# Optimization experiments

Measured on AMD Instinct MI355X. Metric: run time of the kernel, lower is better.

The kernel has to match this reference:

```python
import jax, jax.numpy as jnp
import numpy as np

MAX_CLUSTERS = 5
CLUSTER_SIZE_MAX = 3
K_HOP = 2
TAU = 1.0  # epoch=0 -> tau_init * decay^0 = 1.0
NEG = -1e9


def _logits(x, ctx, W1, b1, W2, b2):
    # x: [B,N,D], ctx: [B,H] -> logits [B,N] (selection_mlp, dropout=eval/identity)
    B, N, _ = x.shape
    h = jnp.concatenate([x, jnp.broadcast_to(ctx[:, None, :], (B, N, ctx.shape[-1]))], axis=-1)
    h = jax.nn.relu(h @ W1.T + b1)
    return (h @ W2.T + b2)[..., 0]


def _select(logits, cand, key):
    # Hard Gumbel-Softmax argmax over candidate nodes; zeros row if no candidates.
    any_c = cand.any(axis=-1, keepdims=True)
    ml = jnp.where(cand, logits, NEG)
    u = jax.random.uniform(key, logits.shape, dtype=logits.dtype)
    g = -jnp.log(-jnp.log(u + 1e-8) + 1e-8)
    idx = jnp.argmax((ml + g) / TAU, axis=-1)
    oh = jax.nn.one_hot(idx, logits.shape[-1], dtype=logits.dtype)
    return oh * any_c.astype(logits.dtype)


def _gru(seq, h0, Wih, Whh, bih, bhh):
    # torch nn.GRU single layer, batch_first; seq: [B,T,D], h0: [B,H] -> final hidden [B,H]
    def cell(h, xt):
        gi = xt @ Wih.T + bih
        gh = h @ Whh.T + bhh
        ir, iz, inn = jnp.split(gi, 3, axis=-1)
        hr, hz, hn = jnp.split(gh, 3, axis=-1)
        r = jax.nn.sigmoid(ir + hr)
        z = jax.nn.sigmoid(iz + hz)
        n = jnp.tanh(inn + r * hn)
        return (1.0 - z) * n + z * h, None
    h, _ = jax.lax.scan(cell, h0, jnp.swapaxes(seq, 0, 1))
    return h


def reference(x, adj, mask, W1, b1, W2, b2, Wc, bc, Wih, Whh, bih, bhh):
    B, N, D = x.shape
    key = jax.random.key(42)
    avail = mask.astype(bool)
    ctx = x.mean(axis=1) @ Wc.T + bc          # context_init  [B,H]
    h_gru = jnp.zeros_like(ctx)               # context_hidden
    assign = jnp.zeros((B, N, MAX_CLUSTERS), x.dtype)
    embs, hist = [], []
    for c in range(MAX_CLUSTERS):
        # logits are identical for every selection within this cluster (same x, same context)
        logits = _logits(x, ctx, W1, b1, W2, b2)  # [B,N]
        # seed selection (torch uses .item() -> selection is a constant index; no grad path)
        seed = jax.lax.stop_gradient(_select(logits, avail, jax.random.fold_in(key, 2 * c)))
        avail = avail & ~(seed > 0.5)
        # k-hop BFS from seed via adjacency matvecs
        reach = seed > 0.5
        cur = seed
        for _ in range(K_HOP):
            nb = jnp.einsum('bn,bnm->bm', cur, adj) > 0
            new = nb & ~reach
            reach = reach | nb
            cur = new.astype(x.dtype)
        member = seed
        for a in range(CLUSTER_SIZE_MAX - 1):
            cand = avail & reach
            sel = jax.lax.stop_gradient(_select(logits, cand, jax.random.fold_in(key, 2 * c + 1000 + a)))
            avail = avail & ~(sel > 0.5)
            member = member + sel
        assign = assign.at[:, :, c].set(member)
        cnt = member.sum(axis=-1, keepdims=True)
        emb = jnp.einsum('bn,bnd->bd', member, x) / jnp.maximum(cnt, 1.0)  # mean of member feats; 0 if empty
        embs.append(emb)
        hist.append(emb)
        # torch re-runs the GRU over the FULL cluster history each iteration, starting
        # from the previously updated hidden state (faithful to the original code)
        h_gru = _gru(jnp.stack(hist, axis=1), h_gru, Wih, Whh, bih, bhh)
        ctx = h_gru
    cluster_features = jnp.stack(embs, axis=1)               # [B,S,D]
    S = MAX_CLUSTERS
    cluster_adj = jnp.ones((B, S, S), x.dtype) - jnp.eye(S, dtype=x.dtype)[None]
    return cluster_features, cluster_adj, assign


def setup_inputs() -> dict:
    key = jax.random.key(0)
    ks = jax.random.split(key, 10)
    B, N, D, H = 16, 2048, 128, 64
    x = jax.random.normal(ks[0], (B, N, D), dtype=jnp.float32)
    # sparse symmetric binary adjacency, ~16 neighbors per node
    a = (jax.random.uniform(ks[1], (B, N, N)) < 0.004).astype(jnp.float32)
    adj = jnp.clip(a + jnp.swapaxes(a, 1, 2), 0.0, 1.0)
    adj = adj * (1.0 - jnp.eye(N, dtype=jnp.float32)[None])
    mask = jnp.ones((B, N), dtype=jnp.int32)
    s = 0.05
    return {
        'x': x, 'adj': adj, 'mask': mask,
        'W1': jax.random.normal(ks[2], (H, D + H)) * s, 'b1': jnp.zeros((H,)),
        'W2': jax.random.normal(ks[3], (1, H)) * s, 'b2': jnp.zeros((1,)),
        'Wc': jax.random.normal(ks[4], (H, D)) * s, 'bc': jnp.zeros((H,)),
        'Wih': jax.random.normal(ks[5], (3 * H, D)) * s,
        'Whh': jax.random.normal(ks[6], (3 * H, H)) * s,
        'bih': jnp.zeros((3 * H,)), 'bhh': jnp.zeros((3 * H,)),
    }
```

## Files before the change

kernel.cpp:

```cpp
#include <hip/hip_runtime.h>
#include <cfloat>
#include <cmath>

#define NB 2048
#define BB 16
#define DD 128
#define HH 64
#define MAXC 5
#define CSMAX 3
#define NT 1024

__device__ __forceinline__ unsigned rotl32(unsigned v, int d) {
  return (v << d) | (v >> (32 - d));
}

__device__ __forceinline__ void tf2x32(unsigned k0, unsigned k1, unsigned x0, unsigned x1,
                                       unsigned& o0, unsigned& o1) {
  unsigned ks2 = k0 ^ k1 ^ 0x1BD11BDAu;
  x0 += k0; x1 += k1;
#define RND(r) { x0 += x1; x1 = rotl32(x1, r); x1 ^= x0; }
  RND(13) RND(15) RND(26) RND(6)   x0 += k1;  x1 += ks2 + 1u;
  RND(17) RND(29) RND(16) RND(24)  x0 += ks2; x1 += k0 + 2u;
  RND(13) RND(15) RND(26) RND(6)   x0 += k0;  x1 += k1 + 3u;
  RND(17) RND(29) RND(16) RND(24)  x0 += k1;  x1 += ks2 + 4u;
  RND(13) RND(15) RND(26) RND(6)   x0 += ks2; x1 += k0 + 5u;
#undef RND
  o0 = x0; o1 = x1;
}

__device__ __forceinline__ float gumbel_for(unsigned k0, unsigned k1, unsigned idx) {
  unsigned o0, o1;
  tf2x32(k0, k1, 0u, idx, o0, o1);
  unsigned bits = o0 ^ o1;
  float u = __uint_as_float((bits >> 9) | 0x3f800000u) - 1.0f;
  float uu = u + 1e-8f;
  return -logf(-logf(uu) + 1e-8f);
}

__global__ __launch_bounds__(NT) void gvp_prep(
    const float* __restrict__ x, const float* __restrict__ W1,
    float* __restrict__ P, float* __restrict__ partial, float* __restrict__ gumb) {
  __shared__ __align__(16) float s_W1[HH][DD + 4];
  __shared__ float sp[8][DD];
  const int bid = blockIdx.x, tid = threadIdx.x;

  if (bid < 128) {
    for (int i = tid; i < HH * (DD / 4); i += NT) {
      int r = i >> 5, q = i & 31;
      *(float4*)&s_W1[r][q * 4] = *(const float4*)(W1 + (size_t)r * (DD + HH) + q * 4);
    }
    __syncthreads();
    const int jg = tid & 15, ng = tid >> 4;
    const int j0 = jg * 4;
    const size_t n0 = (size_t)bid * 256 + ng * 4;
    const float4* x4 = (const float4*)x;
    float acc[4][4];
#pragma unroll
    for (int i = 0; i < 4; i++)
#pragma unroll
      for (int q = 0; q < 4; q++) acc[i][q] = 0.f;
    for (int kq = 0; kq < 32; kq++) {
      float4 xv[4], wv[4];
#pragma unroll
      for (int i = 0; i < 4; i++) xv[i] = x4[(n0 + i) * 32 + kq];
#pragma unroll
      for (int q = 0; q < 4; q++) wv[q] = *(const float4*)&s_W1[j0 + q][kq * 4];
#pragma unroll
      for (int i = 0; i < 4; i++)
#pragma unroll
        for (int q = 0; q < 4; q++)
          acc[i][q] += xv[i].x * wv[q].x + xv[i].y * wv[q].y +
                       xv[i].z * wv[q].z + xv[i].w * wv[q].w;
    }
#pragma unroll
    for (int i = 0; i < 4; i++)
#pragma unroll
      for (int q = 0; q < 4; q++)
        P[(n0 + i) * HH + j0 + q] = acc[i][q];
  } else if (bid < 384) {
    const int bm = bid - 128;
    const int b = bm >> 4, chunk = bm & 15;
    const int d = tid & (DD - 1), part = tid >> 7;
    float acc = 0.f;
    const int base = chunk * 128 + part;
#pragma unroll
    for (int k = 0; k < 16; k++)
      acc += x[((size_t)b * NB + base + k * 8) * DD + d];
    sp[part][d] = acc;
    __syncthreads();
    if (tid < DD) {
      float m = 0.f;
#pragma unroll
      for (int p = 0; p < 8; p++) m += sp[p][tid];
      partial[((size_t)b * 16 + chunk) * DD + tid] = m;
    }
  } else {
    const int bg = bid - 384;
    const int base = (bg * NT + tid) * 4;
#pragma unroll
    for (int i = 0; i < 4; i++) {
      int idx = base + i;
      int sel = idx >> 15;
      int rem = idx & 32767;
      int c = sel / 3, s = sel - 3 * c;
      unsigned data = (s == 0) ? (unsigned)(2 * c) : (unsigned)(2 * c + 1000 + (s - 1));
      unsigned k0, k1;
      tf2x32(0u, 42u, 0u, data, k0, k1);
      gumb[idx] = gumbel_for(k0, k1, (unsigned)rem);
    }
  }
}

__global__ __launch_bounds__(NT, 4) void gvp_main(
    const float* __restrict__ x, const float* __restrict__ adj, const int* __restrict__ mask,
    const float* __restrict__ W1, const float* __restrict__ b1,
    const float* __restrict__ W2, const float* __restrict__ b2,
    const float* __restrict__ Wc, const float* __restrict__ bc,
    const float* __restrict__ Wih, const float* __restrict__ Whh,
    const float* __restrict__ bih, const float* __restrict__ bhh,
    const float* __restrict__ P, const float* __restrict__ partial,
    const float* __restrict__ gumb,
    float* __restrict__ out_feat, float* __restrict__ out_adjm, float* __restrict__ out_assign) {
  const int b = blockIdx.x;
  const int tid = threadIdx.x;

  __shared__ __align__(16) float s_logits[NB];
  __shared__ __align__(16) float s_gumb[2][NB];
  __shared__ unsigned char s_avail[NB], s_reach[NB], s_assignB[NB];
  __shared__ short s_list[128];
  __shared__ int s_cnt;
  __shared__ unsigned long long s_key[CSMAX];
  __shared__ __align__(16) float s_ctx[HH], s_q[HH];
  __shared__ __align__(16) float s_h[2][HH];
  __shared__ __align__(16) float s_hist[MAXC][DD];
  __shared__ __align__(16) float s_giAll[MAXC][3 * HH];
  __shared__ __align__(16) float s_Whh[3 * HH][HH + 4];
  __shared__ __align__(16) float s_W1c[HH][HH + 4];
  __shared__ __align__(16) float s_W2[HH];
  __shared__ float s_bhh[3 * HH], s_b1[HH];
  __shared__ __align__(16) float s_mean[DD];
  __shared__ float s_b2v;

  const size_t xb = (size_t)b * NB * DD;
  const float4* adj4 = (const float4*)(adj + (size_t)b * NB * NB);
  const float4* P4 = (const float4*)(P + (size_t)b * NB * HH);

  auto scanReduce = [&](float bv, int bi, int slot) {
#pragma unroll
    for (int off = 32; off; off >>= 1) {
      float ov = __shfl_down(bv, off);
      int oi = __shfl_down(bi, off);
      if (ov > bv || (ov == bv && oi < bi)) { bv = ov; bi = oi; }
    }
    if ((tid & 63) == 0 && bi < NB) {
      unsigned u = __float_as_uint(bv);
      u = (u & 0x80000000u) ? ~u : (u | 0x80000000u);
      unsigned long long key = ((unsigned long long)u << 32) | (unsigned)(~bi);
      atomicMax(&s_key[slot], key);
    }
  };
  auto decodeIdx = [](unsigned long long k) -> int {
    return k ? (int)(unsigned)(~(unsigned)k) : -1;
  };

  for (int i = tid; i < 3 * HH * (HH / 4); i += NT) {
    int r = i >> 4, q = i & 15;
    *(float4*)&s_Whh[r][q * 4] = *(const float4*)(Whh + (size_t)r * HH + q * 4);
  }
  {
    int r = tid >> 4, q = tid & 15;
    *(float4*)&s_W1c[r][q * 4] = *(const float4*)(W1 + (size_t)r * (DD + HH) + DD + q * 4);
  }
  if (tid < 3 * HH) s_bhh[tid] = bhh[tid];
  if (tid < HH) { s_W2[tid] = W2[tid]; s_b1[tid] = b1[tid]; s_h[0][tid] = 0.f; }
  if (tid == 0) s_b2v = b2[0];
#pragma unroll
  for (int r = 0; r < 2; r++) {
    int n = tid + r * NT;
    s_avail[n] = (mask[b * NB + n] != 0) ? 1 : 0;
    s_assignB[n] = 0;
  }
  if (tid < DD) {
    float m = 0.f;
#pragma unroll
    for (int k = 0; k < 16; k++) m += partial[((size_t)b * 16 + k) * DD + tid];
    s_mean[tid] = m * (1.0f / NB);
  }
  __syncthreads();
  if (tid < 4 * HH) {
    int row = tid >> 2, g = tid & 3;
    const float4* wr = (const float4*)(Wc + (size_t)row * DD) + g * 8;
    const float4* m4 = (const float4*)s_mean + g * 8;
    float s = 0.f;
#pragma unroll
    for (int i = 0; i < 8; i++) {
      float4 w = wr[i], m = m4[i];
      s += w.x * m.x + w.y * m.y + w.z * m.z + w.w * m.w;
    }
    s += __shfl_xor(s, 1);
    s += __shfl_xor(s, 2);
    if (g == 0) s_ctx[row] = s + bc[row];
  }
  __syncthreads();

  int hp = 0;

  for (int c = 0; c < MAXC; c++) {
    const float* g0p = gumb + ((size_t)(c * 3) * BB + b) * NB;
    const float4* g12 = (const float4*)(gumb + ((size_t)(c * 3 + 1 + (tid >> 9)) * BB + b) * NB);
    float4 gst = g12[tid & 511];
    const int n0 = tid, n1 = tid + NT;
    float gs0 = g0p[n0], gs1 = g0p[n1];
    ((float4*)s_gumb)[tid] = gst;
    if (tid < 4 * HH) {
      int row = tid >> 2, g = tid & 3;
      const float4* wr = (const float4*)&s_W1c[row][0] + g * 4;
      const float4* c4 = (const float4*)s_ctx + g * 4;
      float s = 0.f;
#pragma unroll
      for (int i = 0; i < 4; i++) {
        float4 w = wr[i], cc = c4[i];
        s += w.x * cc.x + w.y * cc.y + w.z * cc.z + w.w * cc.w;
      }
      s += __shfl_xor(s, 1);
      s += __shfl_xor(s, 2);
      if (g == 0) s_q[row] = s + s_b1[row];
    }
    if (tid < CSMAX) s_key[tid] = 0ull;
    if (tid == 0) s_cnt = 0;
    __syncthreads();

    {
      float l0 = s_b2v, l1 = s_b2v;
      const float4* p0 = P4 + (size_t)n0 * 16;
      const float4* p1 = P4 + (size_t)n1 * 16;
      const float4* q4 = (const float4*)s_q;
      const float4* w4 = (const float4*)s_W2;
#pragma unroll
      for (int qq = 0; qq < 16; qq += 4) {
        float4 A[4], Bv[4];
#pragma unroll
        for (int i = 0; i < 4; i++) { A[i] = p0[qq + i]; Bv[i] = p1[qq + i]; }
#pragma unroll
        for (int i = 0; i < 4; i++) {
          float4 qv = q4[qq + i], w = w4[qq + i];
          l0 += w.x * fmaxf(A[i].x + qv.x, 0.f) + w.y * fmaxf(A[i].y + qv.y, 0.f) +
                w.z * fmaxf(A[i].z + qv.z, 0.f) + w.w * fmaxf(A[i].w + qv.w, 0.f);
          l1 += w.x * fmaxf(Bv[i].x + qv.x, 0.f) + w.y * fmaxf(Bv[i].y + qv.y, 0.f) +
                w.z * fmaxf(Bv[i].z + qv.z, 0.f) + w.w * fmaxf(Bv[i].w + qv.w, 0.f);
        }
      }
      s_logits[n0] = l0;
      s_logits[n1] = l1;
      float bv = -FLT_MAX;
      int bi = NB;
      if (s_avail[n0]) { float y = l0 + gs0; if (y > bv) { bv = y; bi = n0; } }
      if (s_avail[n1]) { float y = l1 + gs1; if (y > bv || (y == bv && n1 < bi)) { bv = y; bi = n1; } }
      scanReduce(bv, bi, 0);
    }
    __syncthreads();

    const int seed = decodeIdx(s_key[0]);
    if (tid < 512) {
      if (seed >= 0) {
        float4 a = adj4[(size_t)seed * 512 + tid];
        int m = tid << 2;
        unsigned f0 = a.x > 0.f, f1 = a.y > 0.f, f2 = a.z > 0.f, f3 = a.w > 0.f;
        unsigned r = f0 | (f1 << 8) | (f2 << 16) | (f3 << 24);
        if ((seed >> 2) == tid) r |= 1u << ((seed & 3) * 8);
        ((unsigned*)s_reach)[tid] = r;
        if (f0 && m != seed)     { int p = atomicAdd(&s_cnt, 1); if (p < 128) s_list[p] = (short)m; }
        if (f1 && m + 1 != seed) { int p = atomicAdd(&s_cnt, 1); if (p < 128) s_list[p] = (short)(m + 1); }
        if (f2 && m + 2 != seed) { int p = atomicAdd(&s_cnt, 1); if (p < 128) s_list[p] = (short)(m + 2); }
        if (f3 && m + 3 != seed) { int p = atomicAdd(&s_cnt, 1); if (p < 128) s_list[p] = (short)(m + 3); }
      } else {
        ((unsigned*)s_reach)[tid] = 0u;
      }
    }
    __syncthreads();

    if (seed >= 0) {
      int cnt = min(s_cnt, 128);
      int m4 = tid & 511, rg = tid >> 9;
      bool a0 = false, a1 = false, a2 = false, a3 = false;
#pragma unroll
      for (int k = 0; k < 20; k++) {
        int li = rg + 2 * k;
        if (li < cnt) {
          int n = s_list[li];
          float4 a = adj4[(size_t)n * 512 + m4];
          a0 |= a.x > 0.f; a1 |= a.y > 0.f; a2 |= a.z > 0.f; a3 |= a.w > 0.f;
        }
      }
      for (int li = rg + 40; li < cnt; li += 2) {
        int n = s_list[li];
        float4 a = adj4[(size_t)n * 512 + m4];
        a0 |= a.x > 0.f; a1 |= a.y > 0.f; a2 |= a.z > 0.f; a3 |= a.w > 0.f;
      }
      int m = m4 << 2;
      if (a0) s_reach[m] = 1;
      if (a1) s_reach[m + 1] = 1;
      if (a2) s_reach[m + 2] = 1;
      if (a3) s_reach[m + 3] = 1;
    }
    __syncthreads();

    {
      float bv = -FLT_MAX;
      int bi = NB;
#pragma unroll
      for (int r = 0; r < 2; r++) {
        int n = tid + r * NT;
        if (s_avail[n] && s_reach[n] && n != seed) {
          float y = s_logits[n] + s_gumb[0][n];
          if (y > bv || (y == bv && n < bi)) { bv = y; bi = n; }
        }
      }
      scanReduce(bv, bi, 1);
    }
    __syncthreads();

    const int w1i = decodeIdx(s_key[1]);
    {
      float bv = -FLT_MAX;
      int bi = NB;
#pragma unroll
      for (int r = 0; r < 2; r++) {
        int n = tid + r * NT;
        if (s_avail[n] && s_reach[n] && n != seed && n != w1i) {
          float y = s_logits[n] + s_gumb[1][n];
          if (y > bv || (y == bv && n < bi)) { bv = y; bi = n; }
        }
      }
      scanReduce(bv, bi, 2);
    }
    __syncthreads();

    const int w2i = decodeIdx(s_key[2]);
    {
      int mc = (seed >= 0) + (w1i >= 0) + (w2i >= 0);
      if (tid < DD) {
        float acc = 0.f;
        if (seed >= 0) acc += x[xb + (size_t)seed * DD + tid];
        if (w1i >= 0) acc += x[xb + (size_t)w1i * DD + tid];
        if (w2i >= 0) acc += x[xb + (size_t)w2i * DD + tid];
        float e = acc / fmaxf((float)mc, 1.0f);
        s_hist[c][tid] = e;
        out_feat[((size_t)b * MAXC + c) * DD + tid] = e;
      } else if (tid >= 128 && tid < 128 + CSMAX) {
        int idx = (tid == 128) ? seed : (tid == 129 ? w1i : w2i);
        if (idx >= 0) { s_avail[idx] = 0; s_assignB[idx] |= (unsigned char)(1 << c); }
      }
    }
    __syncthreads();

    if (tid < 4 * 3 * HH) {
      int row = tid >> 2, g = tid & 3;
      const float4* wr = (const float4*)(Wih + (size_t)row * DD) + g * 8;
      const float4* h4 = (const float4*)s_hist[c] + g * 8;
      float s = 0.f;
#pragma unroll
      for (int i = 0; i < 8; i++) {
        float4 w = wr[i], hh = h4[i];
        s += w.x * hh.x + w.y * hh.y + w.z * hh.z + w.w * hh.w;
      }
      s += __shfl_xor(s, 1);
      s += __shfl_xor(s, 2);
      if (g == 0) s_giAll[c][row] = s + bih[row];
    }
    __syncthreads();

    for (int t0 = 0; t0 <= c; t0++) {
      if (tid < 4 * HH) {
        int row = tid >> 2, g = tid & 3;
        const float4* h4 = (const float4*)s_h[hp] + g * 4;
        float4 hv[4];
#pragma unroll
        for (int i = 0; i < 4; i++) hv[i] = h4[i];
        const float4* wr = (const float4*)&s_Whh[row][0] + g * 4;
        const float4* wz = (const float4*)&s_Whh[HH + row][0] + g * 4;
        const float4* wn = (const float4*)&s_Whh[2 * HH + row][0] + g * 4;
        float sr = 0.f, sz = 0.f, sn = 0.f;
#pragma unroll
        for (int i = 0; i < 4; i++) {
          float4 a = wr[i], bz = wz[i], cn = wn[i], h = hv[i];
          sr += a.x * h.x + a.y * h.y + a.z * h.z + a.w * h.w;
          sz += bz.x * h.x + bz.y * h.y + bz.z * h.z + bz.w * h.w;
          sn += cn.x * h.x + cn.y * h.y + cn.z * h.z + cn.w * h.w;
        }
        sr += __shfl_xor(sr, 1); sr += __shfl_xor(sr, 2);
        sz += __shfl_xor(sz, 1); sz += __shfl_xor(sz, 2);
        sn += __shfl_xor(sn, 1); sn += __shfl_xor(sn, 2);
        if (g == 0) {
          float r = 1.f / (1.f + expf(-(s_giAll[t0][row] + sr + s_bhh[row])));
          float z = 1.f / (1.f + expf(-(s_giAll[t0][HH + row] + sz + s_bhh[HH + row])));
          float nn = tanhf(s_giAll[t0][2 * HH + row] + r * (sn + s_bhh[2 * HH + row]));
          float hn = (1.f - z) * nn + z * s_h[hp][row];
          s_h[hp ^ 1][row] = hn;
          if (t0 == c) s_ctx[row] = hn;
        }
      }
      hp ^= 1;
      __syncthreads();
    }
  }

#pragma unroll
  for (int r = 0; r < 2; r++) {
    int n = tid + r * NT;
    unsigned bits = s_assignB[n];
    size_t base = ((size_t)(b * NB + n)) * MAXC;
#pragma unroll
    for (int cc = 0; cc < MAXC; cc++)
      out_assign[base + cc] = (float)((bits >> cc) & 1u);
  }
  for (int i = tid; i < MAXC * MAXC; i += NT)
    out_adjm[(size_t)b * MAXC * MAXC + i] = ((i / MAXC) == (i % MAXC)) ? 0.f : 1.f;
}

extern "C" void kernel_launch(void* const* d_in, const int* in_sizes, int n_in,
                              void* d_out, int out_size, void* d_ws, size_t ws_size,
                              hipStream_t stream) {
  const float* x   = (const float*)d_in[0];
  const float* adj = (const float*)d_in[1];
  const int*   mask= (const int*)d_in[2];
  const float* W1  = (const float*)d_in[3];
  const float* b1  = (const float*)d_in[4];
  const float* W2  = (const float*)d_in[5];
  const float* b2  = (const float*)d_in[6];
  const float* Wc  = (const float*)d_in[7];
  const float* bc  = (const float*)d_in[8];
  const float* Wih = (const float*)d_in[9];
  const float* Whh = (const float*)d_in[10];
  const float* bih = (const float*)d_in[11];
  const float* bhh = (const float*)d_in[12];

  float* ws = (float*)d_ws;
  float* P       = ws;
  float* partial = P + (size_t)BB * NB * HH;
  float* gumb    = partial + (size_t)BB * 16 * DD;

  float* out = (float*)d_out;
  float* out_feat = out;
  float* out_adjm = out + (size_t)BB * MAXC * DD;
  float* out_assign = out_adjm + (size_t)BB * MAXC * MAXC;

  hipLaunchKernelGGL(gvp_prep, dim3(504), dim3(NT), 0, stream, x, W1, P, partial, gumb);
  hipLaunchKernelGGL(gvp_main, dim3(BB), dim3(NT), 0, stream,
                     x, adj, mask, W1, b1, W2, b2, Wc, bc, Wih, Whh, bih, bhh, P, partial, gumb,
                     out_feat, out_adjm, out_assign);
}
```

Baseline: 195.0 us.

## Compute Gumbel noise in main kernel and merge member selections into one top-2 pass

The prep kernel no longer precomputes Gumbel noise into a workspace buffer. The main kernel now generates the noise inline with Threefry and computes both member picks in a single pass using a warp top-2 reduction, which removes a block-wide reduction and several barriers per cluster. The GRU input projection is fused with the embedding sum and the per-cluster scaling, and the GRU recurrence runs in a single wavefront using transposed weights. This trades global traffic and synchronisation for extra ALU work and puts the serial GRU steps on 64 threads. The top-2 pass drops the old explicit exclusion of the seed and first pick from the second member's candidates; it relies on the seed already being marked unavailable and on skipping the first pick by index.

Measured after the change: 326.9 us. +67.6%, slower.

```diff
diff --git a/kernel.cpp b/kernel.cpp
--- a/kernel.cpp
+++ b/kernel.cpp
@@ -7,8 +7,10 @@
 #define DD 128
 #define HH 64
 #define MAXC 5
-#define CSMAX 3
 #define NT 1024
+
+#define OFF_P 0
+#define OFF_PART (OFF_P + BB * NB * HH)
 
 __device__ __forceinline__ unsigned rotl32(unsigned v, int d) {
   return (v << d) | (v >> (32 - d));
@@ -37,15 +39,25 @@
   return -logf(-logf(uu) + 1e-8f);
 }
 
-__global__ __launch_bounds__(NT) void gvp_prep(
-    const float* __restrict__ x, const float* __restrict__ W1,
-    float* __restrict__ P, float* __restrict__ partial, float* __restrict__ gumb) {
+__device__ __forceinline__ unsigned long long packKey(float y, int n) {
+  unsigned u = __float_as_uint(y);
+  u = (u & 0x80000000u) ? ~u : (u | 0x80000000u);
+  return ((unsigned long long)u << 32) | (unsigned)(~(unsigned)n);
+}
+__device__ __forceinline__ int decodeKey(unsigned long long k) {
+  return k ? (int)(~(unsigned)k) : -1;
+}
+
+__global__ __launch_bounds__(1024) void gvp_prep(
+    const float* __restrict__ x, const float* __restrict__ W1, float* __restrict__ ws) {
   __shared__ __align__(16) float s_W1[HH][DD + 4];
   __shared__ float sp[8][DD];
   const int bid = blockIdx.x, tid = threadIdx.x;
+  float* P = ws + OFF_P;
+  float* partial = ws + OFF_PART;
 
   if (bid < 128) {
-    for (int i = tid; i < HH * (DD / 4); i += NT) {
+    for (int i = tid; i < HH * (DD / 4); i += 1024) {
       int r = i >> 5, q = i & 31;
       *(float4*)&s_W1[r][q * 4] = *(const float4*)(W1 + (size_t)r * (DD + HH) + q * 4);
     }
@@ -77,7 +89,7 @@
 #pragma unroll
       for (int q = 0; q < 4; q++)
         P[(n0 + i) * HH + j0 + q] = acc[i][q];
-  } else if (bid < 384) {
+  } else {
     const int bm = bid - 128;
     const int b = bm >> 4, chunk = bm & 15;
     const int d = tid & (DD - 1), part = tid >> 7;
@@ -93,20 +105,6 @@
 #pragma unroll
       for (int p = 0; p < 8; p++) m += sp[p][tid];
       partial[((size_t)b * 16 + chunk) * DD + tid] = m;
-    }
-  } else {
-    const int bg = bid - 384;
-    const int base = (bg * NT + tid) * 4;
-#pragma unroll
-    for (int i = 0; i < 4; i++) {
-      int idx = base + i;
-      int sel = idx >> 15;
-      int rem = idx & 32767;
-      int c = sel / 3, s = sel - 3 * c;
-      unsigned data = (s == 0) ? (unsigned)(2 * c) : (unsigned)(2 * c + 1000 + (s - 1));
-      unsigned k0, k1;
-      tf2x32(0u, 42u, 0u, data, k0, k1);
-      gumb[idx] = gumbel_for(k0, k1, (unsigned)rem);
     }
   }
 }
@@ -118,75 +116,54 @@
     const float* __restrict__ Wc, const float* __restrict__ bc,
     const float* __restrict__ Wih, const float* __restrict__ Whh,
     const float* __restrict__ bih, const float* __restrict__ bhh,
-    const float* __restrict__ P, const float* __restrict__ partial,
-    const float* __restrict__ gumb,
+    const float* __restrict__ ws,
     float* __restrict__ out_feat, float* __restrict__ out_adjm, float* __restrict__ out_assign) {
   const int b = blockIdx.x;
   const int tid = threadIdx.x;
-
-  __shared__ __align__(16) float s_logits[NB];
-  __shared__ __align__(16) float s_gumb[2][NB];
-  __shared__ unsigned char s_avail[NB], s_reach[NB], s_assignB[NB];
-  __shared__ short s_list[128];
+  const int t = tid;
+
+  __shared__ float s_WhhT[HH][3 * HH];
+  __shared__ float s_W1cT[HH][HH];
+  __shared__ unsigned char s_avail[NB], s_assignB[NB];
+  __shared__ short s_flist[128];
   __shared__ int s_cnt;
-  __shared__ unsigned long long s_key[CSMAX];
-  __shared__ __align__(16) float s_ctx[HH], s_q[HH];
-  __shared__ __align__(16) float s_h[2][HH];
-  __shared__ __align__(16) float s_hist[MAXC][DD];
+  __shared__ unsigned long long s_key[2];
+  __shared__ unsigned long long s_top2[16][2];
   __shared__ __align__(16) float s_giAll[MAXC][3 * HH];
-  __shared__ __align__(16) float s_Whh[3 * HH][HH + 4];
-  __shared__ __align__(16) float s_W1c[HH][HH + 4];
-  __shared__ __align__(16) float s_W2[HH];
-  __shared__ float s_bhh[3 * HH], s_b1[HH];
+  __shared__ __align__(16) float s_h[HH], s_q[HH], s_ctx[HH];
   __shared__ __align__(16) float s_mean[DD];
+  __shared__ float s_bhh[3 * HH], s_b1[HH], s_W2v[HH];
   __shared__ float s_b2v;
 
+  const size_t adjb = (size_t)b * NB * NB;
   const size_t xb = (size_t)b * NB * DD;
-  const float4* adj4 = (const float4*)(adj + (size_t)b * NB * NB);
-  const float4* P4 = (const float4*)(P + (size_t)b * NB * HH);
-
-  auto scanReduce = [&](float bv, int bi, int slot) {
-#pragma unroll
-    for (int off = 32; off; off >>= 1) {
-      float ov = __shfl_down(bv, off);
-      int oi = __shfl_down(bi, off);
-      if (ov > bv || (ov == bv && oi < bi)) { bv = ov; bi = oi; }
-    }
-    if ((tid & 63) == 0 && bi < NB) {
-      unsigned u = __float_as_uint(bv);
-      u = (u & 0x80000000u) ? ~u : (u | 0x80000000u);
-      unsigned long long key = ((unsigned long long)u << 32) | (unsigned)(~bi);
-      atomicMax(&s_key[slot], key);
-    }
-  };
-  auto decodeIdx = [](unsigned long long k) -> int {
-    return k ? (int)(unsigned)(~(unsigned)k) : -1;
-  };
-
-  for (int i = tid; i < 3 * HH * (HH / 4); i += NT) {
-    int r = i >> 4, q = i & 15;
-    *(float4*)&s_Whh[r][q * 4] = *(const float4*)(Whh + (size_t)r * HH + q * 4);
-  }
-  {
-    int r = tid >> 4, q = tid & 15;
-    *(float4*)&s_W1c[r][q * 4] = *(const float4*)(W1 + (size_t)r * (DD + HH) + DD + q * 4);
+  const float4* P4 = (const float4*)(ws + OFF_P) + (size_t)b * NB * 16;
+
+  for (int f = tid; f < HH * 3 * HH; f += NT) {
+    int k = f / (3 * HH), row = f - k * (3 * HH);
+    s_WhhT[k][row] = Whh[(size_t)row * HH + k];
+  }
+  for (int f = tid; f < HH * HH; f += NT) {
+    int k = f >> 6, row = f & (HH - 1);
+    s_W1cT[k][row] = W1[(size_t)row * (DD + HH) + DD + k];
   }
   if (tid < 3 * HH) s_bhh[tid] = bhh[tid];
-  if (tid < HH) { s_W2[tid] = W2[tid]; s_b1[tid] = b1[tid]; s_h[0][tid] = 0.f; }
+  if (tid >= 256 && tid < 256 + HH) s_b1[tid - 256] = b1[tid - 256];
+  if (tid >= 320 && tid < 320 + HH) s_W2v[tid - 320] = W2[tid - 320];
+  s_avail[t] = (mask[b * NB + t] != 0) ? 1 : 0;
+  s_avail[t + NT] = (mask[b * NB + t + NT] != 0) ? 1 : 0;
+  s_assignB[t] = 0;
+  s_assignB[t + NT] = 0;
+  if (tid >= 384 && tid < 384 + DD) {
+    int d = tid - 384;
+    float m = 0.f;
+#pragma unroll
+    for (int k = 0; k < 16; k++) m += ws[OFF_PART + ((size_t)b * 16 + k) * DD + d];
+    s_mean[d] = m * (1.0f / NB);
+  }
   if (tid == 0) s_b2v = b2[0];
-#pragma unroll
-  for (int r = 0; r < 2; r++) {
-    int n = tid + r * NT;
-    s_avail[n] = (mask[b * NB + n] != 0) ? 1 : 0;
-    s_assignB[n] = 0;
-  }
-  if (tid < DD) {
-    float m = 0.f;
-#pragma unroll
-    for (int k = 0; k < 16; k++) m += partial[((size_t)b * 16 + k) * DD + tid];
-    s_mean[tid] = m * (1.0f / NB);
-  }
   __syncthreads();
+
   if (tid < 4 * HH) {
     int row = tid >> 2, g = tid & 3;
     const float4* wr = (const float4*)(Wc + (size_t)row * DD) + g * 8;
@@ -203,219 +180,224 @@
   }
   __syncthreads();
 
-  int hp = 0;
+  if (tid < 64) {
+    int r = tid;
+    float qs = 0.f;
+    for (int k = 0; k < HH; k += 4) {
+      float4 cv = *(const float4*)&s_ctx[k];
+      qs += s_W1cT[k][r] * cv.x + s_W1cT[k + 1][r] * cv.y +
+            s_W1cT[k + 2][r] * cv.z + s_W1cT[k + 3][r] * cv.w;
+    }
+    s_q[r] = qs + s_b1[r];
+    s_h[r] = 0.f;
+  } else if (tid < 66) s_key[tid - 64] = 0ull;
+  else if (tid < 98) ((unsigned long long*)s_top2)[tid - 66] = 0ull;
+  else if (tid == 98) s_cnt = 0;
+  __syncthreads();
+
+  float l0, l1;
 
   for (int c = 0; c < MAXC; c++) {
-    const float* g0p = gumb + ((size_t)(c * 3) * BB + b) * NB;
-    const float4* g12 = (const float4*)(gumb + ((size_t)(c * 3 + 1 + (tid >> 9)) * BB + b) * NB);
-    float4 gst = g12[tid & 511];
-    const int n0 = tid, n1 = tid + NT;
-    float gs0 = g0p[n0], gs1 = g0p[n1];
-    ((float4*)s_gumb)[tid] = gst;
-    if (tid < 4 * HH) {
-      int row = tid >> 2, g = tid & 3;
-      const float4* wr = (const float4*)&s_W1c[row][0] + g * 4;
-      const float4* c4 = (const float4*)s_ctx + g * 4;
-      float s = 0.f;
-#pragma unroll
-      for (int i = 0; i < 4; i++) {
-        float4 w = wr[i], cc = c4[i];
-        s += w.x * cc.x + w.y * cc.y + w.z * cc.z + w.w * cc.w;
-      }
-      s += __shfl_xor(s, 1);
-      s += __shfl_xor(s, 2);
-      if (g == 0) s_q[row] = s + s_b1[row];
-    }
-    if (tid < CSMAX) s_key[tid] = 0ull;
-    if (tid == 0) s_cnt = 0;
-    __syncthreads();
-
     {
-      float l0 = s_b2v, l1 = s_b2v;
-      const float4* p0 = P4 + (size_t)n0 * 16;
-      const float4* p1 = P4 + (size_t)n1 * 16;
-      const float4* q4 = (const float4*)s_q;
-      const float4* w4 = (const float4*)s_W2;
-#pragma unroll
-      for (int qq = 0; qq < 16; qq += 4) {
-        float4 A[4], Bv[4];
-#pragma unroll
-        for (int i = 0; i < 4; i++) { A[i] = p0[qq + i]; Bv[i] = p1[qq + i]; }
-#pragma unroll
-        for (int i = 0; i < 4; i++) {
-          float4 qv = q4[qq + i], w = w4[qq + i];
-          l0 += w.x * fmaxf(A[i].x + qv.x, 0.f) + w.y * fmaxf(A[i].y + qv.y, 0.f) +
-                w.z * fmaxf(A[i].z + qv.z, 0.f) + w.w * fmaxf(A[i].w + qv.w, 0.f);
-          l1 += w.x * fmaxf(Bv[i].x + qv.x, 0.f) + w.y * fmaxf(Bv[i].y + qv.y, 0.f) +
-                w.z * fmaxf(Bv[i].z + qv.z, 0.f) + w.w * fmaxf(Bv[i].w + qv.w, 0.f);
+      unsigned ka, kb;
+      tf2x32(0u, 42u, 0u, (unsigned)(2 * c), ka, kb);
+      const float4* p0 = P4 + (size_t)t * 16;
+      const float4* p1 = P4 + (size_t)(t + NT) * 16;
+      l0 = s_b2v;
+      l1 = s_b2v;
+#pragma unroll
+      for (int i = 0; i < 16; i++) {
+        float4 pa = p0[i], pb = p1[i];
+        float4 qv = *(const float4*)&s_q[i * 4];
+        float4 w = *(const float4*)&s_W2v[i * 4];
+        l0 += w.x * fmaxf(pa.x + qv.x, 0.f) + w.y * fmaxf(pa.y + qv.y, 0.f) +
+              w.z * fmaxf(pa.z + qv.z, 0.f) + w.w * fmaxf(pa.w + qv.w, 0.f);
+        l1 += w.x * fmaxf(pb.x + qv.x, 0.f) + w.y * fmaxf(pb.y + qv.y, 0.f) +
+              w.z * fmaxf(pb.z + qv.z, 0.f) + w.w * fmaxf(pb.w + qv.w, 0.f);
+      }
+      unsigned long long key = 0ull;
+      if (s_avail[t]) key = packKey(l0 + gumbel_for(ka, kb, (unsigned)(b * NB + t)), t);
+      if (s_avail[t + NT]) {
+        unsigned long long k2 =
+            packKey(l1 + gumbel_for(ka, kb, (unsigned)(b * NB + t + NT)), t + NT);
+        if (k2 > key) key = k2;
+      }
+#pragma unroll
+      for (int off = 32; off; off >>= 1) {
+        unsigned long long o = __shfl_down(key, off);
+        if (o > key) key = o;
+      }
+      if ((tid & 63) == 0 && key) atomicMax(&s_key[0], key);
+    }
+    __syncthreads();
+
+    const int seed = decodeKey(s_key[0]);
+    bool r0 = false, r1 = false;
+    if (seed >= 0) {
+      const float* srow = adj + adjb + (size_t)seed * NB;
+      float a0v = srow[t], a1v = srow[t + NT];
+      r0 = a0v > 0.f;
+      r1 = a1v > 0.f;
+      if (r0) { int p = atomicAdd(&s_cnt, 1); if (p < 128) s_flist[p] = (short)t; }
+      if (r1) { int p = atomicAdd(&s_cnt, 1); if (p < 128) s_flist[p] = (short)(t + NT); }
+      r0 |= (t == seed);
+      r1 |= (t + NT == seed);
+      if (tid == 0) s_avail[seed] = 0;
+    }
+    unsigned k1a, k1b, k2a, k2b;
+    tf2x32(0u, 42u, 0u, (unsigned)(2 * c + 1000), k1a, k1b);
+    tf2x32(0u, 42u, 0u, (unsigned)(2 * c + 1001), k2a, k2b);
+    float g1a = gumbel_for(k1a, k1b, (unsigned)(b * NB + t));
+    float g1b = gumbel_for(k1a, k1b, (unsigned)(b * NB + t + NT));
+    float g2a = gumbel_for(k2a, k2b, (unsigned)(b * NB + t));
+    float g2b = gumbel_for(k2a, k2b, (unsigned)(b * NB + t + NT));
+    __syncthreads();
+
+    if (seed >= 0) {
+      int fc = min(s_cnt, 128);
+      const float* ab = adj + adjb;
+      int fi = 0;
+      for (; fi + 2 <= fc; fi += 2) {
+        int ra = s_flist[fi], rb = s_flist[fi + 1];
+        float a0 = ab[(size_t)ra * NB + t], a1 = ab[(size_t)ra * NB + t + NT];
+        float c0 = ab[(size_t)rb * NB + t], c1 = ab[(size_t)rb * NB + t + NT];
+        r0 |= (a0 > 0.f) | (c0 > 0.f);
+        r1 |= (a1 > 0.f) | (c1 > 0.f);
+      }
+      if (fi < fc) {
+        int ra = s_flist[fi];
+        r0 |= ab[(size_t)ra * NB + t] > 0.f;
+        r1 |= ab[(size_t)ra * NB + t + NT] > 0.f;
+      }
+    }
+    {
+      bool c0 = r0 && s_avail[t], c1 = r1 && s_avail[t + NT];
+      unsigned long long key1 = 0ull, ta = 0ull, tb = 0ull;
+      if (c0) {
+        key1 = packKey(l0 + g1a, t);
+        ta = packKey(l0 + g2a, t);
+      }
+      if (c1) {
+        unsigned long long k = packKey(l1 + g1b, t + NT);
+        if (k > key1) key1 = k;
+        unsigned long long k2 = packKey(l1 + g2b, t + NT);
+        if (k2 > ta) { tb = ta; ta = k2; } else tb = k2;
+      }
+#pragma unroll
+      for (int off = 32; off; off >>= 1) {
+        unsigned long long o = __shfl_down(key1, off);
+        if (o > key1) key1 = o;
+        unsigned long long o1 = __shfl_down(ta, off);
+        unsigned long long o2 = __shfl_down(tb, off);
+        unsigned long long lo = ta < o1 ? ta : o1;
+        unsigned long long hi2 = tb > o2 ? tb : o2;
+        ta = ta > o1 ? ta : o1;
+        tb = lo > hi2 ? lo : hi2;
+      }
+      if ((tid & 63) == 0) {
+        if (key1) atomicMax(&s_key[1], key1);
+        s_top2[tid >> 6][0] = ta;
+        s_top2[tid >> 6][1] = tb;
+      }
+    }
+    __syncthreads();
+
+    const int w1 = decodeKey(s_key[1]);
+    int w2;
+    {
+      unsigned long long t1 = 0ull, t2 = 0ull;
+#pragma unroll
+      for (int i = 0; i < 32; i++) {
+        unsigned long long k = ((unsigned long long*)s_top2)[i];
+        if (k > t1) { t2 = t1; t1 = k; } else if (k > t2) t2 = k;
+      }
+      int i1 = decodeKey(t1);
+      w2 = (i1 == w1) ? decodeKey(t2) : i1;
+    }
+    {
+      int mc = (seed >= 0) + (w1 >= 0) + (w2 >= 0);
+      float invmc = 1.0f / fmaxf((float)mc, 1.0f);
+      if (c < MAXC - 1 && tid < 768) {
+        int row = tid >> 2, g = tid & 3;
+        const float4* wr = (const float4*)(Wih + (size_t)row * DD) + g * 8;
+        const float4* x0 = (seed >= 0) ? (const float4*)(x + xb + (size_t)seed * DD) + g * 8 : nullptr;
+        const float4* x1 = (w1 >= 0) ? (const float4*)(x + xb + (size_t)w1 * DD) + g * 8 : nullptr;
+        const float4* x2 = (w2 >= 0) ? (const float4*)(x + xb + (size_t)w2 * DD) + g * 8 : nullptr;
+        float s = 0.f;
+#pragma unroll
+        for (int i = 0; i < 8; i++) {
+          float4 w = wr[i];
+          float sx = 0.f, sy = 0.f, sz = 0.f, sw = 0.f;
+          if (x0) { float4 v = x0[i]; sx += v.x; sy += v.y; sz += v.z; sw += v.w; }
+          if (x1) { float4 v = x1[i]; sx += v.x; sy += v.y; sz += v.z; sw += v.w; }
+          if (x2) { float4 v = x2[i]; sx += v.x; sy += v.y; sz += v.z; sw += v.w; }
+          s += w.x * sx + w.y * sy + w.z * sz + w.w * sw;
         }
-      }
-      s_logits[n0] = l0;
-      s_logits[n1] = l1;
-      float bv = -FLT_MAX;
-      int bi = NB;
-      if (s_avail[n0]) { float y = l0 + gs0; if (y > bv) { bv = y; bi = n0; } }
-      if (s_avail[n1]) { float y = l1 + gs1; if (y > bv || (y == bv && n1 < bi)) { bv = y; bi = n1; } }
-      scanReduce(bv, bi, 0);
-    }
-    __syncthreads();
-
-    const int seed = decodeIdx(s_key[0]);
-    if (tid < 512) {
-      if (seed >= 0) {
-        float4 a = adj4[(size_t)seed * 512 + tid];
-        int m = tid << 2;
-        unsigned f0 = a.x > 0.f, f1 = a.y > 0.f, f2 = a.z > 0.f, f3 = a.w > 0.f;
-        unsigned r = f0 | (f1 << 8) | (f2 << 16) | (f3 << 24);
-        if ((seed >> 2) == tid) r |= 1u << ((seed & 3) * 8);
-        ((unsigned*)s_reach)[tid] = r;
-        if (f0 && m != seed)     { int p = atomicAdd(&s_cnt, 1); if (p < 128) s_list[p] = (short)m; }
-        if (f1 && m + 1 != seed) { int p = atomicAdd(&s_cnt, 1); if (p < 128) s_list[p] = (short)(m + 1); }
-        if (f2 && m + 2 != seed) { int p = atomicAdd(&s_cnt, 1); if (p < 128) s_list[p] = (short)(m + 2); }
-        if (f3 && m + 3 != seed) { int p = atomicAdd(&s_cnt, 1); if (p < 128) s_list[p] = (short)(m + 3); }
-      } else {
-        ((unsigned*)s_reach)[tid] = 0u;
-      }
-    }
-    __syncthreads();
-
-    if (seed >= 0) {
-      int cnt = min(s_cnt, 128);
-      int m4 = tid & 511, rg = tid >> 9;
-      bool a0 = false, a1 = false, a2 = false, a3 = false;
-#pragma unroll
-      for (int k = 0; k < 20; k++) {
-        int li = rg + 2 * k;
-        if (li < cnt) {
-          int n = s_list[li];
-          float4 a = adj4[(size_t)n * 512 + m4];
-          a0 |= a.x > 0.f; a1 |= a.y > 0.f; a2 |= a.z > 0.f; a3 |= a.w > 0.f;
+        s += __shfl_xor(s, 1);
+        s += __shfl_xor(s, 2);
+        if (g == 0) s_giAll[c][row] = s * invmc + bih[row];
+      }
+      if (tid >= 768 && tid < 768 + DD) {
+        int d = tid - 768;
+        float acc = 0.f;
+        if (seed >= 0) acc += x[xb + (size_t)seed * DD + d];
+        if (w1 >= 0) acc += x[xb + (size_t)w1 * DD + d];
+        if (w2 >= 0) acc += x[xb + (size_t)w2 * DD + d];
+        out_feat[((size_t)b * MAXC + c) * DD + d] = acc * invmc;
+      }
+      if (tid == 896 && seed >= 0) s_assignB[seed] |= (unsigned char)(1 << c);
+      if (tid == 897 && w1 >= 0) { s_assignB[w1] |= (unsigned char)(1 << c); s_avail[w1] = 0; }
+      if (tid == 898 && w2 >= 0) { s_assignB[w2] |= (unsigned char)(1 << c); s_avail[w2] = 0; }
+    }
+    __syncthreads();
+
+    if (c < MAXC - 1) {
+      if (tid < 64) {
+        const int r = tid;
+        float h = s_h[r];
+        for (int tt = 0; tt <= c; tt++) {
+          float sr = 0.f, sz = 0.f, sn = 0.f;
+          for (int k = 0; k < HH; k += 4) {
+            float4 hv = *(const float4*)&s_h[k];
+            sr += s_WhhT[k][r] * hv.x + s_WhhT[k + 1][r] * hv.y +
+                  s_WhhT[k + 2][r] * hv.z + s_WhhT[k + 3][r] * hv.w;
+            sz += s_WhhT[k][HH + r] * hv.x + s_WhhT[k + 1][HH + r] * hv.y +
+                  s_WhhT[k + 2][HH + r] * hv.z + s_WhhT[k + 3][HH + r] * hv.w;
+            sn += s_WhhT[k][2 * HH + r] * hv.x + s_WhhT[k + 1][2 * HH + r] * hv.y +
+                  s_WhhT[k + 2][2 * HH + r] * hv.z + s_WhhT[k + 3][2 * HH + r] * hv.w;
+          }
+          float rr = 1.f / (1.f + expf(-(s_giAll[tt][r] + sr + s_bhh[r])));
+          float zz = 1.f / (1.f + expf(-(s_giAll[tt][HH + r] + sz + s_bhh[HH + r])));
+          float nn = tanhf(s_giAll[tt][2 * HH + r] + rr * (sn + s_bhh[2 * HH + r]));
+          h = (1.f - zz) * nn + zz * h;
+          s_h[r] = h;
         }
-      }
-      for (int li = rg + 40; li < cnt; li += 2) {
-        int n = s_list[li];
-        float4 a = adj4[(size_t)n * 512 + m4];
-        a0 |= a.x > 0.f; a1 |= a.y > 0.f; a2 |= a.z > 0.f; a3 |= a.w > 0.f;
-      }
-      int m = m4 << 2;
-      if (a0) s_reach[m] = 1;
-      if (a1) s_reach[m + 1] = 1;
-      if (a2) s_reach[m + 2] = 1;
-      if (a3) s_reach[m + 3] = 1;
-    }
-    __syncthreads();
-
-    {
-      float bv = -FLT_MAX;
-      int bi = NB;
-#pragma unroll
-      for (int r = 0; r < 2; r++) {
-        int n = tid + r * NT;
-        if (s_avail[n] && s_reach[n] && n != seed) {
-          float y = s_logits[n] + s_gumb[0][n];
-          if (y > bv || (y == bv && n < bi)) { bv = y; bi = n; }
+        float qs = 0.f;
+        for (int k = 0; k < HH; k += 4) {
+          float4 hv = *(const float4*)&s_h[k];
+          qs += s_W1cT[k][r] * hv.x + s_W1cT[k + 1][r] * hv.y +
+                s_W1cT[k + 2][r] * hv.z + s_W1cT[k + 3][r] * hv.w;
         }
-      }
-      scanReduce(bv, bi, 1);
-    }
-    __syncthreads();
-
-    const int w1i = decodeIdx(s_key[1]);
-    {
-      float bv = -FLT_MAX;
-      int bi = NB;
-#pragma unroll
-      for (int r = 0; r < 2; r++) {
-        int n = tid + r * NT;
-        if (s_avail[n] && s_reach[n] && n != seed && n != w1i) {
-          float y = s_logits[n] + s_gumb[1][n];
-          if (y > bv || (y == bv && n < bi)) { bv = y; bi = n; }
-        }
-      }
-      scanReduce(bv, bi, 2);
-    }
-    __syncthreads();
-
-    const int w2i = decodeIdx(s_key[2]);
-    {
-      int mc = (seed >= 0) + (w1i >= 0) + (w2i >= 0);
-      if (tid < DD) {
-        float acc = 0.f;
-        if (seed >= 0) acc += x[xb + (size_t)seed * DD + tid];
-        if (w1i >= 0) acc += x[xb + (size_t)w1i * DD + tid];
-        if (w2i >= 0) acc += x[xb + (size_t)w2i * DD + tid];
-        float e = acc / fmaxf((float)mc, 1.0f);
-        s_hist[c][tid] = e;
-        out_feat[((size_t)b * MAXC + c) * DD + tid] = e;
-      } else if (tid >= 128 && tid < 128 + CSMAX) {
-        int idx = (tid == 128) ? seed : (tid == 129 ? w1i : w2i);
-        if (idx >= 0) { s_avail[idx] = 0; s_assignB[idx] |= (unsigned char)(1 << c); }
-      }
-    }
-    __syncthreads();
-
-    if (tid < 4 * 3 * HH) {
-      int row = tid >> 2, g = tid & 3;
-      const float4* wr = (const float4*)(Wih + (size_t)row * DD) + g * 8;
-      const float4* h4 = (const float4*)s_hist[c] + g * 8;
-      float s = 0.f;
-#pragma unroll
-      for (int i = 0; i < 8; i++) {
-        float4 w = wr[i], hh = h4[i];
-        s += w.x * hh.x + w.y * hh.y + w.z * hh.z + w.w * hh.w;
-      }
-      s += __shfl_xor(s, 1);
-      s += __shfl_xor(s, 2);
-      if (g == 0) s_giAll[c][row] = s + bih[row];
-    }
-    __syncthreads();
-
-    for (int t0 = 0; t0 <= c; t0++) {
-      if (tid < 4 * HH) {
-        int row = tid >> 2, g = tid & 3;
-        const float4* h4 = (const float4*)s_h[hp] + g * 4;
-        float4 hv[4];
-#pragma unroll
-        for (int i = 0; i < 4; i++) hv[i] = h4[i];
-        const float4* wr = (const float4*)&s_Whh[row][0] + g * 4;
-        const float4* wz = (const float4*)&s_Whh[HH + row][0] + g * 4;
-        const float4* wn = (const float4*)&s_Whh[2 * HH + row][0] + g * 4;
-        float sr = 0.f, sz = 0.f, sn = 0.f;
-#pragma unroll
-        for (int i = 0; i < 4; i++) {
-          float4 a = wr[i], bz = wz[i], cn = wn[i], h = hv[i];
-          sr += a.x * h.x + a.y * h.y + a.z * h.z + a.w * h.w;
-          sz += bz.x * h.x + bz.y * h.y + bz.z * h.z + bz.w * h.w;
-          sn += cn.x * h.x + cn.y * h.y + cn.z * h.z + cn.w * h.w;
-        }
-        sr += __shfl_xor(sr, 1); sr += __shfl_xor(sr, 2);
-        sz += __shfl_xor(sz, 1); sz += __shfl_xor(sz, 2);
-        sn += __shfl_xor(sn, 1); sn += __shfl_xor(sn, 2);
-        if (g == 0) {
-          float r = 1.f / (1.f + expf(-(s_giAll[t0][row] + sr + s_bhh[row])));
-          float z = 1.f / (1.f + expf(-(s_giAll[t0][HH + row] + sz + s_bhh[HH + row])));
-          float nn = tanhf(s_giAll[t0][2 * HH + row] + r * (sn + s_bhh[2 * HH + row]));
-          float hn = (1.f - z) * nn + z * s_h[hp][row];
-          s_h[hp ^ 1][row] = hn;
-          if (t0 == c) s_ctx[row] = hn;
-        }
-      }
-      hp ^= 1;
+        s_q[r] = qs + s_b1[r];
+      } else if (tid < 66) s_key[tid - 64] = 0ull;
+      else if (tid < 98) ((unsigned long long*)s_top2)[tid - 66] = 0ull;
+      else if (tid == 98) s_cnt = 0;
       __syncthreads();
     }
   }
 
 #pragma unroll
-  for (int r = 0; r < 2; r++) {
-    int n = tid + r * NT;
+  for (int rr = 0; rr < 2; rr++) {
+    int n = t + rr * NT;
     unsigned bits = s_assignB[n];
-    size_t base = ((size_t)(b * NB + n)) * MAXC;
+    size_t basei = ((size_t)(b * NB + n)) * MAXC;
 #pragma unroll
     for (int cc = 0; cc < MAXC; cc++)
-      out_assign[base + cc] = (float)((bits >> cc) & 1u);
-  }
-  for (int i = tid; i < MAXC * MAXC; i += NT)
+      out_assign[basei + cc] = (float)((bits >> cc) & 1u);
+  }
+  for (int i = tid; i < MAXC * MAXC; i += NT) {
     out_adjm[(size_t)b * MAXC * MAXC + i] = ((i / MAXC) == (i % MAXC)) ? 0.f : 1.f;
+  }
 }
 
 extern "C" void kernel_launch(void* const* d_in, const int* in_sizes, int n_in,
@@ -436,17 +418,13 @@
   const float* bhh = (const float*)d_in[12];
 
   float* ws = (float*)d_ws;
-  float* P       = ws;
-  float* partial = P + (size_t)BB * NB * HH;
-  float* gumb    = partial + (size_t)BB * 16 * DD;
-
   float* out = (float*)d_out;
   float* out_feat = out;
   float* out_adjm = out + (size_t)BB * MAXC * DD;
   float* out_assign = out_adjm + (size_t)BB * MAXC * MAXC;
 
-  hipLaunchKernelGGL(gvp_prep, dim3(504), dim3(NT), 0, stream, x, W1, P, partial, gumb);
+  hipLaunchKernelGGL(gvp_prep, dim3(384), dim3(1024), 0, stream, x, W1, ws);
   hipLaunchKernelGGL(gvp_main, dim3(BB), dim3(NT), 0, stream,
-                     x, adj, mask, W1, b1, W2, b2, Wc, bc, Wih, Whh, bih, bhh, P, partial, gumb,
+                     x, adj, mask, W1, b1, W2, b2, Wc, bc, Wih, Whh, bih, bhh, ws,
                      out_feat, out_adjm, out_assign);
 }
```
